# Optimization experiments

Hardware: AMD Instinct MI355X
Metric: run time of the kernel (lower is better)

The kernel has to match this reference:

```python
import jax, jax.numpy as jnp
import numpy as np

NEG_SLOPE = 0.2
N_NODES = 50000


def gat_conv(x, src, dst, W, a_src, a_dst, b, n_nodes):
    """One PyG-style GATConv layer (eval mode, self-loops already in src/dst).
    x: [N, F_in]; W: [F_in, H*C]; a_src/a_dst: [H, C]; b: [H*C] or [C].
    Returns per-node, per-head outputs [N, H, C].
    """
    H, C = a_src.shape
    h = (x @ W).reshape(-1, H, C)                      # [N, H, C]
    s_src = jnp.sum(h * a_src[None], axis=-1)          # [N, H]
    s_dst = jnp.sum(h * a_dst[None], axis=-1)          # [N, H]
    e = jax.nn.leaky_relu(s_src[src] + s_dst[dst], NEG_SLOPE)   # [E, H]
    # segment softmax over incoming edges of each destination node
    m = jax.ops.segment_max(e, dst, num_segments=n_nodes)       # [N, H]
    w = jnp.exp(e - m[dst])                                     # [E, H]
    denom = jax.ops.segment_sum(w, dst, num_segments=n_nodes)   # [N, H]
    alpha = w / denom[dst]                                      # [E, H]
    # weighted aggregation of source features
    out = jax.ops.segment_sum(alpha[:, :, None] * h[src], dst, num_segments=n_nodes)
    return out  # [N, H, C]


def setup_inputs() -> dict:
    key = jax.random.key(0)
    ks = jax.random.split(key, 12)
    N, F_in, Hid, H, F_out = N_NODES, 128, 64, 4, 128
    E = 800000
    x = jax.random.normal(ks[0], (N, F_in), dtype=jnp.float32)
    edge_index = jax.random.randint(ks[1], (2, E), 0, N, dtype=jnp.int64)
    sc = 0.1
    return {
        "x": x,
        "edge_index": edge_index,
        "W1": jax.random.normal(ks[2], (F_in, H * Hid), dtype=jnp.float32) * sc,
        "att_src1": jax.random.normal(ks[3], (H, Hid), dtype=jnp.float32) * sc,
        "att_dst1": jax.random.normal(ks[4], (H, Hid), dtype=jnp.float32) * sc,
        "b1": jnp.zeros((H * Hid,), dtype=jnp.float32),
        "W2": jax.random.normal(ks[5], (H * Hid, F_out), dtype=jnp.float32) * sc,
        "att_src2": jax.random.normal(ks[6], (1, F_out), dtype=jnp.float32) * sc,
        "att_dst2": jax.random.normal(ks[7], (1, F_out), dtype=jnp.float32) * sc,
        "b2": jnp.zeros((F_out,), dtype=jnp.float32),
    }


def reference(x, edge_index, W1, att_src1, att_dst1, b1, W2, att_src2, att_dst2, b2):
    N = x.shape[0]
    # PyG GATConv adds self-loops by default
    loops = jnp.arange(N, dtype=edge_index.dtype)
    src = jnp.concatenate([edge_index[0], loops])
    dst = jnp.concatenate([edge_index[1], loops])
    # layer 1: heads=4, concat -> [N, H*Hid], then ELU (dropout is identity in eval)
    h1 = gat_conv(x, src, dst, W1, att_src1, att_dst1, b1, N)    # [N, H, Hid]
    h1 = h1.reshape(N, -1) + b1
    h1 = jax.nn.elu(h1)
    # layer 2: heads=1, concat=False -> mean over the single head
    h2 = gat_conv(h1, src, dst, W2, att_src2, att_dst2, b2, N)   # [N, 1, F_out]
    out = h2[:, 0, :] + b2
    return out
```

## Files before the change

kernel.cpp:

```cpp
#include <hip/hip_runtime.h>
#include <cmath>

typedef __attribute__((ext_vector_type(8))) short bf16x8;
typedef __attribute__((ext_vector_type(4))) float f32x4;

static __device__ __forceinline__ unsigned short f2bf(float f) {
    unsigned u = __float_as_uint(f);
    unsigned r = (u + 0x7fffu + ((u >> 16) & 1u)) >> 16;
    return (unsigned short)r;
}
static __device__ __forceinline__ unsigned packbf(float a, float b) {
    return (unsigned)f2bf(a) | ((unsigned)f2bf(b) << 16);
}
static __device__ __forceinline__ float bflo(unsigned u) { return __uint_as_float(u << 16); }
static __device__ __forceinline__ float bfhi(unsigned u) { return __uint_as_float(u & 0xffff0000u); }

__global__ void prep_k(const float* __restrict__ x, const float* __restrict__ W1,
                       const float* __restrict__ W2, unsigned* __restrict__ xb,
                       unsigned short* __restrict__ Wt1, unsigned short* __restrict__ Wt2,
                       int* __restrict__ deg, int NX2, int NW1, int NW2, int N) {
    int i = blockIdx.x * blockDim.x + threadIdx.x;
    if (i < NX2) {
        float2 v = reinterpret_cast<const float2*>(x)[i];
        xb[i] = packbf(v.x, v.y);
        return;
    }
    i -= NX2;
    if (i < NW1) { int nn = i / 128, k = i % 128; Wt1[i] = f2bf(W1[(size_t)k * 256 + nn]); return; }
    i -= NW1;
    if (i < NW2) { int nn = i / 256, k = i % 256; Wt2[i] = f2bf(W2[(size_t)k * 128 + nn]); return; }
    i -= NW2;
    if (i < N) deg[i] = 1;
}

__global__ void count_k(const int* __restrict__ dst, int E, int* __restrict__ deg) {
    int e = blockIdx.x * blockDim.x + threadIdx.x;
    if (e < E) atomicAdd(&deg[dst[e]], 1);
}

#define SCAN_BLK 256
#define SCAN_ELEMS 2048

__global__ void scan1_k(const int* __restrict__ deg, int* __restrict__ rowstart,
                        int* __restrict__ bsums, int N) {
    __shared__ int sh[SCAN_BLK];
    int t = threadIdx.x;
    int base = blockIdx.x * SCAN_ELEMS + t * 8;
    int vals[8];
    int sum = 0;
#pragma unroll
    for (int i = 0; i < 8; ++i) {
        int idx = base + i;
        vals[i] = (idx < N) ? deg[idx] : 0;
        sum += vals[i];
    }
    sh[t] = sum;
    __syncthreads();
    for (int off = 1; off < SCAN_BLK; off <<= 1) {
        int v = (t >= off) ? sh[t - off] : 0;
        __syncthreads();
        sh[t] += v;
        __syncthreads();
    }
    int run = sh[t] - sum;
    if (t == SCAN_BLK - 1) bsums[blockIdx.x] = sh[t];
#pragma unroll
    for (int i = 0; i < 8; ++i) {
        int idx = base + i;
        if (idx < N) rowstart[idx] = run;
        run += vals[i];
    }
}
__global__ void scan2_k(int* __restrict__ bsums, int nb) {
    if (threadIdx.x == 0 && blockIdx.x == 0) {
        int run = 0;
        for (int i = 0; i < nb; ++i) { int t = bsums[i]; bsums[i] = run; run += t; }
    }
}
__global__ void scan3_init_k(int* __restrict__ rowstart, const int* __restrict__ bsums,
                             int* __restrict__ adj, int* __restrict__ cursor, int N, int total) {
    int i = blockIdx.x * blockDim.x + threadIdx.x;
    if (i < N) {
        int r = rowstart[i] + bsums[i / SCAN_ELEMS];
        rowstart[i] = r;
        adj[r] = i;
        cursor[i] = r + 1;
    } else if (i == N) {
        rowstart[N] = total;
    }
}
__global__ void scatter_k(const int* __restrict__ src, const int* __restrict__ dst, int E,
                          int* __restrict__ cursor, int* __restrict__ adj) {
    int e = blockIdx.x * blockDim.x + threadIdx.x;
    if (e >= E) return;
    int pos = atomicAdd(&cursor[dst[e]], 1);
    adj[pos] = src[e];
}

template<int K, int NOUT>
__global__ __launch_bounds__(256) void gemm_mfma_k(const unsigned* __restrict__ Ab,
                                                   const unsigned* __restrict__ Bt,
                                                   unsigned short* __restrict__ Yb, int N) {
    __shared__ unsigned short As[128 * 64];
    __shared__ unsigned short Bs[64 * 64];
    int tid = threadIdx.x;
    int lane = tid & 63, wid = tid >> 6;
    int wm = wid >> 1, wc = wid & 1;
    int m0 = blockIdx.x * 128;
    int n0 = blockIdx.y * 64;

    f32x4 acc[4][2] = {};

    for (int k0 = 0; k0 < K; k0 += 64) {
#pragma unroll
        for (int p = 0; p < 4; ++p) {
            int gl = p * 256 + tid;
            int row = gl >> 3, g = gl & 7;
            int grow = m0 + row; if (grow >= N) grow = N - 1;
            uint4 v = *reinterpret_cast<const uint4*>(Ab + (size_t)grow * (K / 2) + k0 / 2 + g * 4);
            *reinterpret_cast<uint4*>((char*)As + row * 128 + ((g ^ (row & 7)) << 4)) = v;
        }
#pragma unroll
        for (int p = 0; p < 2; ++p) {
            int gl = p * 256 + tid;
            int row = gl >> 3, g = gl & 7;
            uint4 v = *reinterpret_cast<const uint4*>(Bt + (size_t)(n0 + row) * (K / 2) + k0 / 2 + g * 4);
            *reinterpret_cast<uint4*>((char*)Bs + row * 128 + ((g ^ (row & 7)) << 4)) = v;
        }
        __syncthreads();

        bf16x8 bfrag[2][2];
#pragma unroll
        for (int kk = 0; kk < 2; ++kk)
#pragma unroll
            for (int no = 0; no < 2; ++no) {
                int row = wc * 32 + no * 16 + (lane & 15);
                int g = kk * 4 + (lane >> 4);
                bfrag[kk][no] = *reinterpret_cast<const bf16x8*>((char*)Bs + row * 128 + ((g ^ (row & 7)) << 4));
            }
#pragma unroll
        for (int mo = 0; mo < 4; ++mo) {
#pragma unroll
            for (int kk = 0; kk < 2; ++kk) {
                int row = wm * 64 + mo * 16 + (lane & 15);
                int g = kk * 4 + (lane >> 4);
                bf16x8 afrag = *reinterpret_cast<const bf16x8*>((char*)As + row * 128 + ((g ^ (row & 7)) << 4));
                acc[mo][0] = __builtin_amdgcn_mfma_f32_16x16x32_bf16(afrag, bfrag[kk][0], acc[mo][0], 0, 0, 0);
                acc[mo][1] = __builtin_amdgcn_mfma_f32_16x16x32_bf16(afrag, bfrag[kk][1], acc[mo][1], 0, 0, 0);
            }
        }
        __syncthreads();
    }
#pragma unroll
    for (int mo = 0; mo < 4; ++mo)
#pragma unroll
        for (int no = 0; no < 2; ++no) {
            int col = n0 + wc * 32 + no * 16 + (lane & 15);
            int rbase = m0 + wm * 64 + mo * 16 + (lane >> 4) * 4;
#pragma unroll
            for (int j = 0; j < 4; ++j) {
                int row = rbase + j;
                if (row < N) Yb[(size_t)row * NOUT + col] = f2bf(acc[mo][no][j]);
            }
        }
}

template<int H, int C>
__global__ void score_b_k(const unsigned* __restrict__ hb, const float* __restrict__ a_src,
                          const float* __restrict__ a_dst,
                          float* __restrict__ ssrc, float* __restrict__ sdst, int N) {
    int idx = blockIdx.x * blockDim.x + threadIdx.x;
    if (idx >= N * H) return;
    int n = idx / H, hh = idx % H;
    const uint4* hp = reinterpret_cast<const uint4*>(hb + (size_t)n * (H * C / 2) + hh * (C / 2));
    const float* as = a_src + hh * C;
    const float* ad = a_dst + hh * C;
    float ss = 0.f, sd = 0.f;
#pragma unroll
    for (int i = 0; i < C / 8; ++i) {
        uint4 u = hp[i];
        float v[8] = {bflo(u.x), bfhi(u.x), bflo(u.y), bfhi(u.y),
                      bflo(u.z), bfhi(u.z), bflo(u.w), bfhi(u.w)};
#pragma unroll
        for (int j = 0; j < 8; ++j) { ss += v[j] * as[i * 8 + j]; sd += v[j] * ad[i * 8 + j]; }
    }
    ssrc[idx] = ss;
    sdst[idx] = sd;
}

template<int H, int C, bool ELU, bool OUT_BF16>
__global__ void node_agg_k(const int* __restrict__ rowstart, const int* __restrict__ adj,
                           const float* __restrict__ ssrc, const float* __restrict__ sdst,
                           const unsigned* __restrict__ hb, const float* __restrict__ bias,
                           void* __restrict__ outp, int N) {
    constexpr int HC = H * C;
    constexpr int ROW_U = HC / 2;
    constexpr int ULN = ROW_U / 32;
    constexpr int FPLn = ULN * 2;
    int lane = threadIdx.x & 63;
    int w = threadIdx.x >> 6;
    int n = blockIdx.x * (blockDim.x >> 6) + w;
    if (n >= N) return;

    __shared__ int   s_sh[4][64];
    __shared__ float a_sh[4][64 * H];

    int r0 = rowstart[n], r1 = rowstart[n + 1];
    int deg = r1 - r0;

    float sd[H];
#pragma unroll
    for (int h = 0; h < H; ++h) sd[h] = sdst[n * H + h];

    if (deg <= 64) {
        int s = adj[r0 + ((lane < deg) ? lane : 0)];
        float a[H];
        {
            float v[H];
            if constexpr (H == 4) {
                float4 sv = reinterpret_cast<const float4*>(ssrc)[s];
                v[0] = sv.x; v[1] = sv.y; v[2] = sv.z; v[3] = sv.w;
            } else {
                v[0] = ssrc[s];
            }
#pragma unroll
            for (int h = 0; h < H; ++h) {
                float t = v[h] + sd[h];
                t = t > 0.f ? t : 0.2f * t;
                v[h] = (lane < deg) ? t : -1e30f;
            }
            float m[H], l[H];
#pragma unroll
            for (int h = 0; h < H; ++h) m[h] = v[h];
#pragma unroll
            for (int off = 32; off; off >>= 1)
#pragma unroll
                for (int h = 0; h < H; ++h)
                    m[h] = fmaxf(m[h], __shfl_xor(m[h], off, 64));
#pragma unroll
            for (int h = 0; h < H; ++h) {
                a[h] = (lane < deg) ? __expf(v[h] - m[h]) : 0.f;
                l[h] = a[h];
            }
#pragma unroll
            for (int off = 32; off; off >>= 1)
#pragma unroll
                for (int h = 0; h < H; ++h)
                    l[h] += __shfl_xor(l[h], off, 64);
#pragma unroll
            for (int h = 0; h < H; ++h) a[h] *= __builtin_amdgcn_rcpf(l[h]);
        }
        s_sh[w][lane] = s;
#pragma unroll
        for (int h = 0; h < H; ++h) a_sh[w][lane * H + h] = a[h];

        int ln = lane & 31, half = lane >> 5;
        int hA = (ln * FPLn) / C;
        const unsigned* hbl = hb + ln * ULN;
        float acc[FPLn];
#pragma unroll
        for (int f = 0; f < FPLn; ++f) acc[f] = 0.f;

        int j = half;
        for (; j + 6 < deg; j += 8) {
            int s0 = s_sh[w][j],     s1 = s_sh[w][j + 2];
            int s2 = s_sh[w][j + 4], s3 = s_sh[w][j + 6];
            float al0 = a_sh[w][j * H + hA],       al1 = a_sh[w][(j + 2) * H + hA];
            float al2 = a_sh[w][(j + 4) * H + hA], al3 = a_sh[w][(j + 6) * H + hA];
            if constexpr (ULN == 4) {
                uint4 u0 = *reinterpret_cast<const uint4*>(hbl + (size_t)s0 * ROW_U);
                uint4 u1 = *reinterpret_cast<const uint4*>(hbl + (size_t)s1 * ROW_U);
                uint4 u2 = *reinterpret_cast<const uint4*>(hbl + (size_t)s2 * ROW_U);
                uint4 u3 = *reinterpret_cast<const uint4*>(hbl + (size_t)s3 * ROW_U);
                acc[0] += al0 * bflo(u0.x); acc[1] += al0 * bfhi(u0.x);
                acc[2] += al0 * bflo(u0.y); acc[3] += al0 * bfhi(u0.y);
                acc[4] += al0 * bflo(u0.z); acc[5] += al0 * bfhi(u0.z);
                acc[6] += al0 * bflo(u0.w); acc[7] += al0 * bfhi(u0.w);
                acc[0] += al1 * bflo(u1.x); acc[1] += al1 * bfhi(u1.x);
                acc[2] += al1 * bflo(u1.y); acc[3] += al1 * bfhi(u1.y);
                acc[4] += al1 * bflo(u1.z); acc[5] += al1 * bfhi(u1.z);
                acc[6] += al1 * bflo(u1.w); acc[7] += al1 * bfhi(u1.w);
                acc[0] += al2 * bflo(u2.x); acc[1] += al2 * bfhi(u2.x);
                acc[2] += al2 * bflo(u2.y); acc[3] += al2 * bfhi(u2.y);
                acc[4] += al2 * bflo(u2.z); acc[5] += al2 * bfhi(u2.z);
                acc[6] += al2 * bflo(u2.w); acc[7] += al2 * bfhi(u2.w);
                acc[0] += al3 * bflo(u3.x); acc[1] += al3 * bfhi(u3.x);
                acc[2] += al3 * bflo(u3.y); acc[3] += al3 * bfhi(u3.y);
                acc[4] += al3 * bflo(u3.z); acc[5] += al3 * bfhi(u3.z);
                acc[6] += al3 * bflo(u3.w); acc[7] += al3 * bfhi(u3.w);
            } else {
                uint2 u0 = *reinterpret_cast<const uint2*>(hbl + (size_t)s0 * ROW_U);
                uint2 u1 = *reinterpret_cast<const uint2*>(hbl + (size_t)s1 * ROW_U);
                uint2 u2 = *reinterpret_cast<const uint2*>(hbl + (size_t)s2 * ROW_U);
                uint2 u3 = *reinterpret_cast<const uint2*>(hbl + (size_t)s3 * ROW_U);
                acc[0] += al0 * bflo(u0.x); acc[1] += al0 * bfhi(u0.x);
                acc[2] += al0 * bflo(u0.y); acc[3] += al0 * bfhi(u0.y);
                acc[0] += al1 * bflo(u1.x); acc[1] += al1 * bfhi(u1.x);
                acc[2] += al1 * bflo(u1.y); acc[3] += al1 * bfhi(u1.y);
                acc[0] += al2 * bflo(u2.x); acc[1] += al2 * bfhi(u2.x);
                acc[2] += al2 * bflo(u2.y); acc[3] += al2 * bfhi(u2.y);
                acc[0] += al3 * bflo(u3.x); acc[1] += al3 * bfhi(u3.x);
                acc[2] += al3 * bflo(u3.y); acc[3] += al3 * bfhi(u3.y);
            }
        }
        for (; j < deg; j += 2) {
            int sj = s_sh[w][j];
            float al = a_sh[w][j * H + hA];
            if constexpr (ULN == 4) {
                uint4 u = *reinterpret_cast<const uint4*>(hbl + (size_t)sj * ROW_U);
                acc[0] += al * bflo(u.x); acc[1] += al * bfhi(u.x);
                acc[2] += al * bflo(u.y); acc[3] += al * bfhi(u.y);
                acc[4] += al * bflo(u.z); acc[5] += al * bfhi(u.z);
                acc[6] += al * bflo(u.w); acc[7] += al * bfhi(u.w);
            } else {
                uint2 u = *reinterpret_cast<const uint2*>(hbl + (size_t)sj * ROW_U);
                acc[0] += al * bflo(u.x); acc[1] += al * bfhi(u.x);
                acc[2] += al * bflo(u.y); acc[3] += al * bfhi(u.y);
            }
        }
#pragma unroll
        for (int f = 0; f < FPLn; ++f) acc[f] += __shfl_xor(acc[f], 32, 64);
#pragma unroll
        for (int f = 0; f < FPLn; ++f) {
            float v = acc[f] + bias[ln * FPLn + f];
            if (ELU) v = v > 0.f ? v : (__expf(v) - 1.f);
            acc[f] = v;
        }
        if (half == 0) {
            if constexpr (OUT_BF16) {
                unsigned* op = (unsigned*)outp + (size_t)n * ROW_U + ln * ULN;
                if constexpr (ULN == 4) {
                    uint4 u = {packbf(acc[0], acc[1]), packbf(acc[2], acc[3]),
                               packbf(acc[4], acc[5]), packbf(acc[6], acc[7])};
                    *reinterpret_cast<uint4*>(op) = u;
                } else {
                    uint2 u = {packbf(acc[0], acc[1]), packbf(acc[2], acc[3])};
                    *reinterpret_cast<uint2*>(op) = u;
                }
            } else {
                float* op = (float*)outp + (size_t)n * HC + ln * FPLn;
                if constexpr (FPLn == 4) {
                    *reinterpret_cast<float4*>(op) = make_float4(acc[0], acc[1], acc[2], acc[3]);
                } else {
#pragma unroll
                    for (int f = 0; f < FPLn; ++f) op[f] = acc[f];
                }
            }
        }
    } else {
        constexpr int FPL = HC / 64;
        constexpr int UPL = FPL / 2;
        int hA = (lane * FPL) / C;
        float acc[FPL];
#pragma unroll
        for (int f = 0; f < FPL; ++f) acc[f] = 0.f;
        float m[H], l[H];
#pragma unroll
        for (int h = 0; h < H; ++h) { m[h] = -1e30f; l[h] = 0.f; }
        for (int e = r0 + lane; e < r1; e += 64) {
            int s = adj[e];
#pragma unroll
            for (int h = 0; h < H; ++h) {
                float v = ssrc[s * H + h] + sd[h];
                v = v > 0.f ? v : 0.2f * v;
                float mn = fmaxf(m[h], v);
                l[h] = l[h] * __expf(m[h] - mn) + __expf(v - mn);
                m[h] = mn;
            }
        }
#pragma unroll
        for (int off = 32; off; off >>= 1)
#pragma unroll
            for (int h = 0; h < H; ++h) {
                float mo = __shfl_xor(m[h], off, 64);
                float lo = __shfl_xor(l[h], off, 64);
                float mn = fmaxf(m[h], mo);
                l[h] = l[h] * __expf(m[h] - mn) + lo * __expf(mo - mn);
                m[h] = mn;
            }
        float mh = m[hA], invl = 1.f / l[hA], sdh = sd[hA];
        for (int e = r0; e < r1; ++e) {
            int s = adj[e];
            float v = ssrc[s * H + hA] + sdh;
            v = v > 0.f ? v : 0.2f * v;
            float alpha = __expf(v - mh) * invl;
            const unsigned* hp = hb + (size_t)s * ROW_U + lane * UPL;
            if constexpr (UPL == 2) {
                uint2 u = *reinterpret_cast<const uint2*>(hp);
                acc[0] += alpha * bflo(u.x); acc[1] += alpha * bfhi(u.x);
                acc[2] += alpha * bflo(u.y); acc[3] += alpha * bfhi(u.y);
            } else {
                unsigned u = *hp;
                acc[0] += alpha * bflo(u); acc[1] += alpha * bfhi(u);
            }
        }
#pragma unroll
        for (int f = 0; f < FPL; ++f) {
            float v = acc[f] + bias[lane * FPL + f];
            if (ELU) v = v > 0.f ? v : (__expf(v) - 1.f);
            acc[f] = v;
        }
        if constexpr (OUT_BF16) {
            unsigned* op = (unsigned*)outp + (size_t)n * ROW_U + lane * UPL;
            if constexpr (UPL == 2) {
                uint2 u = {packbf(acc[0], acc[1]), packbf(acc[2], acc[3])};
                *reinterpret_cast<uint2*>(op) = u;
            } else {
                *op = packbf(acc[0], acc[1]);
            }
        } else {
            float* op = (float*)outp + (size_t)n * HC + lane * FPL;
#pragma unroll
            for (int f = 0; f < FPL; ++f) op[f] = acc[f];
        }
    }
}

extern "C" void kernel_launch(void* const* d_in, const int* in_sizes, int n_in,
                              void* d_out, int out_size, void* d_ws, size_t ws_size,
                              hipStream_t stream) {
    const float* x   = (const float*)d_in[0];
    const int*   ei  = (const int*)d_in[1];
    const float* W1  = (const float*)d_in[2];
    const float* as1 = (const float*)d_in[3];
    const float* ad1 = (const float*)d_in[4];
    const float* b1  = (const float*)d_in[5];
    const float* W2  = (const float*)d_in[6];
    const float* as2 = (const float*)d_in[7];
    const float* ad2 = (const float*)d_in[8];
    const float* b2  = (const float*)d_in[9];
    float* out = (float*)d_out;

    const int N  = in_sizes[0] / 128;
    const int E  = in_sizes[1] / 2;
    const int ET = E + N;
    const int* src = ei;
    const int* dst = ei + E;

    unsigned* ws = (unsigned*)d_ws;
    unsigned* xb    = ws;
    unsigned* h1b   = xb    + (size_t)N * 64;
    unsigned* agg1b = h1b   + (size_t)N * 128;
    unsigned* h2b   = agg1b + (size_t)N * 128;
    unsigned* Wt1   = h2b   + (size_t)N * 64;
    unsigned* Wt2   = Wt1   + 16384;
    float*    ssrc1 = (float*)(Wt2 + 16384);
    float*    sdst1 = ssrc1 + (size_t)N * 4;
    float*    ssrc2 = sdst1 + (size_t)N * 4;
    float*    sdst2 = ssrc2 + N;
    int*      deg   = (int*)(sdst2 + N);
    int*      rowst = deg + N;
    int*      bsums = rowst + N + 1;
    int*      adj   = bsums + 64;

    const int B = 256;
    auto blocks = [](size_t n, int b) { return (int)((n + b - 1) / b); };
    const int nscan = (N + SCAN_ELEMS - 1) / SCAN_ELEMS;

    {
        int NX2 = N * 64, NW1 = 128 * 256, NW2 = 256 * 128;
        size_t tot = (size_t)NX2 + NW1 + NW2 + N;
        prep_k<<<blocks(tot, B), B, 0, stream>>>(x, W1, W2, xb, (unsigned short*)Wt1,
                                                 (unsigned short*)Wt2, deg, NX2, NW1, NW2, N);
    }

    count_k<<<blocks(E, B), B, 0, stream>>>(dst, E, deg);
    scan1_k<<<nscan, SCAN_BLK, 0, stream>>>(deg, rowst, bsums, N);
    scan2_k<<<1, 64, 0, stream>>>(bsums, nscan);
    scan3_init_k<<<blocks(N + 1, B), B, 0, stream>>>(rowst, bsums, adj, deg, N, ET);
    scatter_k<<<blocks(E, B), B, 0, stream>>>(src, dst, E, deg, adj);

    {
        dim3 g((N + 127) / 128, 256 / 64);
        gemm_mfma_k<128, 256><<<g, 256, 0, stream>>>(xb, (const unsigned*)Wt1, (unsigned short*)h1b, N);
    }
    score_b_k<4, 64><<<blocks((size_t)N * 4, B), B, 0, stream>>>(h1b, as1, ad1, ssrc1, sdst1, N);
    node_agg_k<4, 64, true, true><<<(N + 3) / 4, 256, 0, stream>>>(rowst, adj, ssrc1, sdst1, h1b, b1, agg1b, N);

    {
        dim3 g((N + 127) / 128, 128 / 64);
        gemm_mfma_k<256, 128><<<g, 256, 0, stream>>>(agg1b, (const unsigned*)Wt2, (unsigned short*)h2b, N);
    }
    score_b_k<1, 128><<<blocks(N, B), B, 0, stream>>>(h2b, as2, ad2, ssrc2, sdst2, N);
    node_agg_k<1, 128, false, false><<<(N + 3) / 4, 256, 0, stream>>>(rowst, adj, ssrc2, sdst2, h2b, b2, out, N);
}
```

Measured before the change: 275.1 us.

## Fuse degree count into prep, warp-scan block sums, drop softmax max, regroup aggregation

Degree counting moves into the prep kernel after a memset, and the self-loop is added during the scan instead of by an initial fill. This removes one launch. The block-sum scan now runs as a 64-lane shuffle scan rather than a single-thread loop. In the low-degree path the segment-softmax max reduction is dropped and raw exponentials are normalized directly, which risks overflow for large logits. The aggregation loop is parameterized by lane group size so layer 2 uses 16-lane groups with 128-bit loads, processing four edges in parallel per wave.

```diff
diff --git a/kernel.cpp b/kernel.cpp
--- a/kernel.cpp
+++ b/kernel.cpp
@@ -16,9 +16,10 @@
 static __device__ __forceinline__ float bfhi(unsigned u) { return __uint_as_float(u & 0xffff0000u); }
 
 __global__ void prep_k(const float* __restrict__ x, const float* __restrict__ W1,
-                       const float* __restrict__ W2, unsigned* __restrict__ xb,
+                       const float* __restrict__ W2, const int* __restrict__ dst,
+                       unsigned* __restrict__ xb,
                        unsigned short* __restrict__ Wt1, unsigned short* __restrict__ Wt2,
-                       int* __restrict__ deg, int NX2, int NW1, int NW2, int N) {
+                       int* __restrict__ deg, int NX2, int NW1, int NW2, int E) {
     int i = blockIdx.x * blockDim.x + threadIdx.x;
     if (i < NX2) {
         float2 v = reinterpret_cast<const float2*>(x)[i];
@@ -30,12 +31,7 @@
     i -= NW1;
     if (i < NW2) { int nn = i / 256, k = i % 256; Wt2[i] = f2bf(W2[(size_t)k * 128 + nn]); return; }
     i -= NW2;
-    if (i < N) deg[i] = 1;
-}
-
-__global__ void count_k(const int* __restrict__ dst, int E, int* __restrict__ deg) {
-    int e = blockIdx.x * blockDim.x + threadIdx.x;
-    if (e < E) atomicAdd(&deg[dst[e]], 1);
+    if (i < E) atomicAdd(&deg[dst[i]], 1);
 }
 
 #define SCAN_BLK 256
@@ -51,7 +47,7 @@
 #pragma unroll
     for (int i = 0; i < 8; ++i) {
         int idx = base + i;
-        vals[i] = (idx < N) ? deg[idx] : 0;
+        vals[i] = (idx < N) ? (deg[idx] + 1) : 0;
         sum += vals[i];
     }
     sh[t] = sum;
@@ -72,10 +68,14 @@
     }
 }
 __global__ void scan2_k(int* __restrict__ bsums, int nb) {
-    if (threadIdx.x == 0 && blockIdx.x == 0) {
-        int run = 0;
-        for (int i = 0; i < nb; ++i) { int t = bsums[i]; bsums[i] = run; run += t; }
-    }
+    int lane = threadIdx.x;
+    int own = (lane < nb) ? bsums[lane] : 0;
+    int v = own;
+    for (int off = 1; off < 64; off <<= 1) {
+        int t = __shfl_up(v, off, 64);
+        if (lane >= off) v += t;
+    }
+    if (lane < nb) bsums[lane] = v - own;
 }
 __global__ void scan3_init_k(int* __restrict__ rowstart, const int* __restrict__ bsums,
                              int* __restrict__ adj, int* __restrict__ cursor, int N, int total) {
@@ -188,15 +188,16 @@
     sdst[idx] = sd;
 }
 
-template<int H, int C, bool ELU, bool OUT_BF16>
+template<int H, int C, int GRP, bool ELU, bool OUT_BF16>
 __global__ void node_agg_k(const int* __restrict__ rowstart, const int* __restrict__ adj,
                            const float* __restrict__ ssrc, const float* __restrict__ sdst,
                            const unsigned* __restrict__ hb, const float* __restrict__ bias,
                            void* __restrict__ outp, int N) {
     constexpr int HC = H * C;
     constexpr int ROW_U = HC / 2;
-    constexpr int ULN = ROW_U / 32;
+    constexpr int ULN = ROW_U / GRP;
     constexpr int FPLn = ULN * 2;
+    constexpr int NGRP = 64 / GRP;
     int lane = threadIdx.x & 63;
     int w = threadIdx.x >> 6;
     int n = blockIdx.x * (blockDim.x >> 6) + w;
@@ -214,7 +215,7 @@
 
     if (deg <= 64) {
         int s = adj[r0 + ((lane < deg) ? lane : 0)];
-        float a[H];
+        float a[H], l[H];
         {
             float v[H];
             if constexpr (H == 4) {
@@ -227,26 +228,16 @@
             for (int h = 0; h < H; ++h) {
                 float t = v[h] + sd[h];
                 t = t > 0.f ? t : 0.2f * t;
-                v[h] = (lane < deg) ? t : -1e30f;
-            }
-            float m[H], l[H];
-#pragma unroll
-            for (int h = 0; h < H; ++h) m[h] = v[h];
-#pragma unroll
-            for (int off = 32; off; off >>= 1)
-#pragma unroll
-                for (int h = 0; h < H; ++h)
-                    m[h] = fmaxf(m[h], __shfl_xor(m[h], off, 64));
-#pragma unroll
-            for (int h = 0; h < H; ++h) {
-                a[h] = (lane < deg) ? __expf(v[h] - m[h]) : 0.f;
+                a[h] = (lane < deg) ? __expf(t) : 0.f;
                 l[h] = a[h];
             }
-#pragma unroll
-            for (int off = 32; off; off >>= 1)
-#pragma unroll
-                for (int h = 0; h < H; ++h)
-                    l[h] += __shfl_xor(l[h], off, 64);
+            if (deg > 32)
+#pragma unroll
+                for (int h = 0; h < H; ++h) l[h] += __shfl_xor(l[h], 32, 64);
+#pragma unroll
+            for (int off = 16; off; off >>= 1)
+#pragma unroll
+                for (int h = 0; h < H; ++h) l[h] += __shfl_xor(l[h], off, 64);
 #pragma unroll
             for (int h = 0; h < H; ++h) a[h] *= __builtin_amdgcn_rcpf(l[h]);
         }
@@ -254,97 +245,69 @@
 #pragma unroll
         for (int h = 0; h < H; ++h) a_sh[w][lane * H + h] = a[h];
 
-        int ln = lane & 31, half = lane >> 5;
+        int g = lane / GRP, ln = lane % GRP;
         int hA = (ln * FPLn) / C;
         const unsigned* hbl = hb + ln * ULN;
         float acc[FPLn];
 #pragma unroll
         for (int f = 0; f < FPLn; ++f) acc[f] = 0.f;
 
-        int j = half;
-        for (; j + 6 < deg; j += 8) {
-            int s0 = s_sh[w][j],     s1 = s_sh[w][j + 2];
-            int s2 = s_sh[w][j + 4], s3 = s_sh[w][j + 6];
-            float al0 = a_sh[w][j * H + hA],       al1 = a_sh[w][(j + 2) * H + hA];
-            float al2 = a_sh[w][(j + 4) * H + hA], al3 = a_sh[w][(j + 6) * H + hA];
-            if constexpr (ULN == 4) {
-                uint4 u0 = *reinterpret_cast<const uint4*>(hbl + (size_t)s0 * ROW_U);
-                uint4 u1 = *reinterpret_cast<const uint4*>(hbl + (size_t)s1 * ROW_U);
-                uint4 u2 = *reinterpret_cast<const uint4*>(hbl + (size_t)s2 * ROW_U);
-                uint4 u3 = *reinterpret_cast<const uint4*>(hbl + (size_t)s3 * ROW_U);
-                acc[0] += al0 * bflo(u0.x); acc[1] += al0 * bfhi(u0.x);
-                acc[2] += al0 * bflo(u0.y); acc[3] += al0 * bfhi(u0.y);
-                acc[4] += al0 * bflo(u0.z); acc[5] += al0 * bfhi(u0.z);
-                acc[6] += al0 * bflo(u0.w); acc[7] += al0 * bfhi(u0.w);
-                acc[0] += al1 * bflo(u1.x); acc[1] += al1 * bfhi(u1.x);
-                acc[2] += al1 * bflo(u1.y); acc[3] += al1 * bfhi(u1.y);
-                acc[4] += al1 * bflo(u1.z); acc[5] += al1 * bfhi(u1.z);
-                acc[6] += al1 * bflo(u1.w); acc[7] += al1 * bfhi(u1.w);
-                acc[0] += al2 * bflo(u2.x); acc[1] += al2 * bfhi(u2.x);
-                acc[2] += al2 * bflo(u2.y); acc[3] += al2 * bfhi(u2.y);
-                acc[4] += al2 * bflo(u2.z); acc[5] += al2 * bfhi(u2.z);
-                acc[6] += al2 * bflo(u2.w); acc[7] += al2 * bfhi(u2.w);
-                acc[0] += al3 * bflo(u3.x); acc[1] += al3 * bfhi(u3.x);
-                acc[2] += al3 * bflo(u3.y); acc[3] += al3 * bfhi(u3.y);
-                acc[4] += al3 * bflo(u3.z); acc[5] += al3 * bfhi(u3.z);
-                acc[6] += al3 * bflo(u3.w); acc[7] += al3 * bfhi(u3.w);
-            } else {
-                uint2 u0 = *reinterpret_cast<const uint2*>(hbl + (size_t)s0 * ROW_U);
-                uint2 u1 = *reinterpret_cast<const uint2*>(hbl + (size_t)s1 * ROW_U);
-                uint2 u2 = *reinterpret_cast<const uint2*>(hbl + (size_t)s2 * ROW_U);
-                uint2 u3 = *reinterpret_cast<const uint2*>(hbl + (size_t)s3 * ROW_U);
-                acc[0] += al0 * bflo(u0.x); acc[1] += al0 * bfhi(u0.x);
-                acc[2] += al0 * bflo(u0.y); acc[3] += al0 * bfhi(u0.y);
-                acc[0] += al1 * bflo(u1.x); acc[1] += al1 * bfhi(u1.x);
-                acc[2] += al1 * bflo(u1.y); acc[3] += al1 * bfhi(u1.y);
-                acc[0] += al2 * bflo(u2.x); acc[1] += al2 * bfhi(u2.x);
-                acc[2] += al2 * bflo(u2.y); acc[3] += al2 * bfhi(u2.y);
-                acc[0] += al3 * bflo(u3.x); acc[1] += al3 * bfhi(u3.x);
-                acc[2] += al3 * bflo(u3.y); acc[3] += al3 * bfhi(u3.y);
-            }
-        }
-        for (; j < deg; j += 2) {
+        int j = g;
+        for (; j + 3 * NGRP < deg; j += 4 * NGRP) {
+            int s0 = s_sh[w][j],            s1 = s_sh[w][j + NGRP];
+            int s2 = s_sh[w][j + 2 * NGRP], s3 = s_sh[w][j + 3 * NGRP];
+            float al0 = a_sh[w][j * H + hA],            al1 = a_sh[w][(j + NGRP) * H + hA];
+            float al2 = a_sh[w][(j + 2 * NGRP) * H + hA], al3 = a_sh[w][(j + 3 * NGRP) * H + hA];
+            uint4 u0 = *reinterpret_cast<const uint4*>(hbl + (size_t)s0 * ROW_U);
+            uint4 u1 = *reinterpret_cast<const uint4*>(hbl + (size_t)s1 * ROW_U);
+            uint4 u2 = *reinterpret_cast<const uint4*>(hbl + (size_t)s2 * ROW_U);
+            uint4 u3 = *reinterpret_cast<const uint4*>(hbl + (size_t)s3 * ROW_U);
+            acc[0] += al0 * bflo(u0.x); acc[1] += al0 * bfhi(u0.x);
+            acc[2] += al0 * bflo(u0.y); acc[3] += al0 * bfhi(u0.y);
+            acc[4] += al0 * bflo(u0.z); acc[5] += al0 * bfhi(u0.z);
+            acc[6] += al0 * bflo(u0.w); acc[7] += al0 * bfhi(u0.w);
+            acc[0] += al1 * bflo(u1.x); acc[1] += al1 * bfhi(u1.x);
+            acc[2] += al1 * bflo(u1.y); acc[3] += al1 * bfhi(u1.y);
+            acc[4] += al1 * bflo(u1.z); acc[5] += al1 * bfhi(u1.z);
+            acc[6] += al1 * bflo(u1.w); acc[7] += al1 * bfhi(u1.w);
+            acc[0] += al2 * bflo(u2.x); acc[1] += al2 * bfhi(u2.x);
+            acc[2] += al2 * bflo(u2.y); acc[3] += al2 * bfhi(u2.y);
+            acc[4] += al2 * bflo(u2.z); acc[5] += al2 * bfhi(u2.z);
+            acc[6] += al2 * bflo(u2.w); acc[7] += al2 * bfhi(u2.w);
+            acc[0] += al3 * bflo(u3.x); acc[1] += al3 * bfhi(u3.x);
+            acc[2] += al3 * bflo(u3.y); acc[3] += al3 * bfhi(u3.y);
+            acc[4] += al3 * bflo(u3.z); acc[5] += al3 * bfhi(u3.z);
+            acc[6] += al3 * bflo(u3.w); acc[7] += al3 * bfhi(u3.w);
+        }
+        for (; j < deg; j += NGRP) {
             int sj = s_sh[w][j];
             float al = a_sh[w][j * H + hA];
-            if constexpr (ULN == 4) {
-                uint4 u = *reinterpret_cast<const uint4*>(hbl + (size_t)sj * ROW_U);
-                acc[0] += al * bflo(u.x); acc[1] += al * bfhi(u.x);
-                acc[2] += al * bflo(u.y); acc[3] += al * bfhi(u.y);
-                acc[4] += al * bflo(u.z); acc[5] += al * bfhi(u.z);
-                acc[6] += al * bflo(u.w); acc[7] += al * bfhi(u.w);
-            } else {
-                uint2 u = *reinterpret_cast<const uint2*>(hbl + (size_t)sj * ROW_U);
-                acc[0] += al * bflo(u.x); acc[1] += al * bfhi(u.x);
-                acc[2] += al * bflo(u.y); acc[3] += al * bfhi(u.y);
-            }
-        }
-#pragma unroll
-        for (int f = 0; f < FPLn; ++f) acc[f] += __shfl_xor(acc[f], 32, 64);
+            uint4 u = *reinterpret_cast<const uint4*>(hbl + (size_t)sj * ROW_U);
+            acc[0] += al * bflo(u.x); acc[1] += al * bfhi(u.x);
+            acc[2] += al * bflo(u.y); acc[3] += al * bfhi(u.y);
+            acc[4] += al * bflo(u.z); acc[5] += al * bfhi(u.z);
+            acc[6] += al * bflo(u.w); acc[7] += al * bfhi(u.w);
+        }
+#pragma unroll
+        for (int off = GRP; off < 64; off <<= 1)
+#pragma unroll
+            for (int f = 0; f < FPLn; ++f) acc[f] += __shfl_xor(acc[f], off, 64);
 #pragma unroll
         for (int f = 0; f < FPLn; ++f) {
             float v = acc[f] + bias[ln * FPLn + f];
             if (ELU) v = v > 0.f ? v : (__expf(v) - 1.f);
             acc[f] = v;
         }
-        if (half == 0) {
+        if (g == 0) {
             if constexpr (OUT_BF16) {
                 unsigned* op = (unsigned*)outp + (size_t)n * ROW_U + ln * ULN;
-                if constexpr (ULN == 4) {
-                    uint4 u = {packbf(acc[0], acc[1]), packbf(acc[2], acc[3]),
-                               packbf(acc[4], acc[5]), packbf(acc[6], acc[7])};
-                    *reinterpret_cast<uint4*>(op) = u;
-                } else {
-                    uint2 u = {packbf(acc[0], acc[1]), packbf(acc[2], acc[3])};
-                    *reinterpret_cast<uint2*>(op) = u;
-                }
+                uint4 u = {packbf(acc[0], acc[1]), packbf(acc[2], acc[3]),
+                           packbf(acc[4], acc[5]), packbf(acc[6], acc[7])};
+                *reinterpret_cast<uint4*>(op) = u;
             } else {
                 float* op = (float*)outp + (size_t)n * HC + ln * FPLn;
-                if constexpr (FPLn == 4) {
-                    *reinterpret_cast<float4*>(op) = make_float4(acc[0], acc[1], acc[2], acc[3]);
-                } else {
-#pragma unroll
-                    for (int f = 0; f < FPLn; ++f) op[f] = acc[f];
-                }
+                *reinterpret_cast<float4*>(op) = make_float4(acc[0], acc[1], acc[2], acc[3]);
+                *reinterpret_cast<float4*>(op + 4) = make_float4(acc[4], acc[5], acc[6], acc[7]);
             }
         }
     } else {
@@ -457,14 +420,14 @@
     auto blocks = [](size_t n, int b) { return (int)((n + b - 1) / b); };
     const int nscan = (N + SCAN_ELEMS - 1) / SCAN_ELEMS;
 
+    hipMemsetAsync(deg, 0, (size_t)N * 4, stream);
     {
         int NX2 = N * 64, NW1 = 128 * 256, NW2 = 256 * 128;
-        size_t tot = (size_t)NX2 + NW1 + NW2 + N;
-        prep_k<<<blocks(tot, B), B, 0, stream>>>(x, W1, W2, xb, (unsigned short*)Wt1,
-                                                 (unsigned short*)Wt2, deg, NX2, NW1, NW2, N);
-    }
-
-    count_k<<<blocks(E, B), B, 0, stream>>>(dst, E, deg);
+        size_t tot = (size_t)NX2 + NW1 + NW2 + E;
+        prep_k<<<blocks(tot, B), B, 0, stream>>>(x, W1, W2, dst, xb, (unsigned short*)Wt1,
+                                                 (unsigned short*)Wt2, deg, NX2, NW1, NW2, E);
+    }
+
     scan1_k<<<nscan, SCAN_BLK, 0, stream>>>(deg, rowst, bsums, N);
     scan2_k<<<1, 64, 0, stream>>>(bsums, nscan);
     scan3_init_k<<<blocks(N + 1, B), B, 0, stream>>>(rowst, bsums, adj, deg, N, ET);
@@ -475,12 +438,12 @@
         gemm_mfma_k<128, 256><<<g, 256, 0, stream>>>(xb, (const unsigned*)Wt1, (unsigned short*)h1b, N);
     }
     score_b_k<4, 64><<<blocks((size_t)N * 4, B), B, 0, stream>>>(h1b, as1, ad1, ssrc1, sdst1, N);
-    node_agg_k<4, 64, true, true><<<(N + 3) / 4, 256, 0, stream>>>(rowst, adj, ssrc1, sdst1, h1b, b1, agg1b, N);
+    node_agg_k<4, 64, 32, true, true><<<(N + 3) / 4, 256, 0, stream>>>(rowst, adj, ssrc1, sdst1, h1b, b1, agg1b, N);
 
     {
         dim3 g((N + 127) / 128, 128 / 64);
         gemm_mfma_k<256, 128><<<g, 256, 0, stream>>>(agg1b, (const unsigned*)Wt2, (unsigned short*)h2b, N);
     }
     score_b_k<1, 128><<<blocks(N, B), B, 0, stream>>>(h2b, as2, ad2, ssrc2, sdst2, N);
-    node_agg_k<1, 128, false, false><<<(N + 3) / 4, 256, 0, stream>>>(rowst, adj, ssrc2, sdst2, h2b, b2, out, N);
-}
+    node_agg_k<1, 128, 16, false, false><<<(N + 3) / 4, 256, 0, stream>>>(rowst, adj, ssrc2, sdst2, h2b, b2, out, N);
+}
```

Result: faster. 262.4 us (-4.6%).
